# Kernel tuning notes

Hardware: AMD Instinct MI355X
Metric: run time of the kernel (lower is better)

Reference implementation:

```python
import jax, jax.numpy as jnp
import numpy as np

B = 8          # batch_size
N = 2048       # N_particles
D_SP = 2       # spatial dims
D = 16         # D_SP + hidden_dim
K = 32         # max_num_neighbors
R = 0.08       # neighbor_radius
DT = 0.01      # leapfrog step
BIG = 1e9


def setup_inputs() -> dict:
    key = jax.random.key(0)
    ks = jax.random.split(key, 8)
    H, C = 64, 32
    # node state: small random hidden features, deterministic disk positions
    x = jax.random.normal(ks[0], (B * N, D), dtype=jnp.float32) * 0.001
    i = jnp.arange(N, dtype=jnp.float32)
    golden = jnp.pi * (3.0 - jnp.sqrt(5.0))
    theta = i * golden
    r = 0.6 * jnp.sqrt((i + 0.5) / N)
    pos = jnp.stack([r * jnp.cos(theta), r * jnp.sin(theta)], axis=1)  # [N,2]
    pos = jnp.tile(pos, (B, 1)) + 0.01 * jax.random.normal(ks[1], (B * N, 2), dtype=jnp.float32)
    x = x.at[:, :D_SP].set(pos)
    W1 = jax.random.normal(ks[2], (2 * D, H), dtype=jnp.float32) * (1.0 / np.sqrt(2 * D))
    b1 = jnp.zeros((H,), jnp.float32)
    W2 = jax.random.normal(ks[3], (H, C), dtype=jnp.float32) * (1.0 / np.sqrt(H))
    b2 = jnp.zeros((C,), jnp.float32)
    Wout = jax.random.normal(ks[4], (C, 1), dtype=jnp.float32) * (1.0 / np.sqrt(C))
    bout = jnp.zeros((1,), jnp.float32)
    batch = jnp.repeat(jnp.arange(B, dtype=jnp.int64), N)
    return {"x": x, "W1": W1, "b1": b1, "W2": W2, "b2": b2,
            "Wout": Wout, "bout": bout, "batch": batch, "steps": 2}


def reference(x, W1, b1, W2, b2, Wout, bout, batch, steps):
    Bn, Df = x.shape
    Bc = int(np.asarray(batch)[-1]) + 1      # batch is contiguous blocks
    Nn = Bn // Bc
    eye = jnp.eye(Nn, dtype=x.dtype) * BIG   # no self-loops (loop=False)

    def hamiltonian(xv):
        xb = xv.reshape(Bc, Nn, Df)
        pos = xb[:, :, :D_SP]                              # [B,N,2]
        # radius_graph: pairwise sq-dist per simulation, capped at K neighbors
        d2 = jnp.sum((pos[:, :, None, :] - pos[:, None, :, :]) ** 2, axis=-1)  # [B,N,N]
        d2 = d2 + eye
        negd, idx = jax.lax.top_k(-d2, K)                  # K nearest per node
        valid = (-negd) < (R * R)                          # [B,N,K]
        # gather neighbor states (HNNConv message on concat(x_i, x_j))
        xj = xb[jnp.arange(Bc)[:, None, None], idx]        # [B,N,K,D]
        xi = jnp.broadcast_to(xb[:, :, None, :], xj.shape)
        m = jnp.tanh(jnp.concatenate([xi, xj], axis=-1) @ W1 + b1)  # [B,N,K,H]
        m = m @ W2 + b2                                    # [B,N,K,C]
        m = jnp.where(valid[..., None], m, 0.0)
        agg = m.sum(axis=2)                                # sum aggregation [B,N,C]
        h = agg @ Wout + bout                              # per-node Hamiltonian [B,N,1]
        return h.sum()

    for _ in range(int(steps)):
        dHdx = jax.grad(hamiltonian)(x)
        x = x - DT * dHdx
    return x
```

## Files before the change

kernel.cpp:

```cpp
#include <hip/hip_runtime.h>
#include <cstdint>
#include <cstddef>

#define BB   8
#define NN   2048
#define DD   16
#define HHH  64
#define KK   32
#define CAP  96
#define DT_C 0.01f
#define R2_C (0.08f * 0.08f)
#define CEXP (-2.885390081777927f)

#define WPB   16
#define BLOCK (WPB * 64)

__device__ __forceinline__ float dist2(float px, float py, float qx, float qy) {
    float dx = __fsub_rn(px, qx);
    float dy = __fsub_rn(py, qy);
    return __fadd_rn(__fmul_rn(dx, dx), __fmul_rn(dy, dy));
}

__device__ __forceinline__ int mbcnt64(unsigned long long m) {
    return (int)__builtin_amdgcn_mbcnt_hi(
        (unsigned)(m >> 32), __builtin_amdgcn_mbcnt_lo((unsigned)m, 0u));
}

__device__ __forceinline__ int swizzled_particle(int blk, int w, int& bbase) {
    int vb = blk & 7, vi = blk >> 3;
    bbase = vb << 11;
    return bbase + vi * WPB + w;
}

template <bool FIRST>
__global__ __launch_bounds__(BLOCK) void k_neighbors(
    const float* __restrict__ x, const float* __restrict__ pos,
    const float* __restrict__ W1,
    unsigned short* __restrict__ nbr, int* __restrict__ cntArr,
    float* __restrict__ cutArr,
    float* __restrict__ Aplane, float* __restrict__ Dplane) {
    __shared__ float sPos[2 * NN];
    __shared__ float sW1[2 * DD * HHH];
    __shared__ float2 sDJ[WPB][CAP];

    int tid = threadIdx.x;
    int w = tid >> 6, lane = tid & 63;
    int bbase;
    int p = swizzled_particle(blockIdx.x, w, bbase);
    int pl = p & (NN - 1);

    float2* sPos2w = (float2*)sPos;
    if (FIRST) {
        for (int t = tid; t < NN; t += BLOCK)
            sPos2w[t] = *(const float2*)(x + (size_t)(bbase + t) * DD);
    } else {
        for (int t = tid; t < 2 * NN; t += BLOCK) sPos[t] = pos[bbase * 2 + t];
    }
    for (int t = tid; t < 2 * DD * HHH; t += BLOCK) sW1[t] = W1[t];
    __syncthreads();

    float xv = (lane < DD) ? x[(size_t)p * DD + lane] : 0.f;
    float A = 0.f, Dv = 0.f;
#pragma unroll
    for (int f = 0; f < DD; f++) {
        float xf = __shfl(xv, f);
        A  = fmaf(xf, sW1[f * HHH + lane], A);
        Dv = fmaf(xf, sW1[(DD + f) * HHH + lane], Dv);
    }
    Aplane[((size_t)p << 6) + lane] = A;
    Dplane[((size_t)p << 6) + lane] = Dv;

    float px = sPos[2 * pl], py = sPos[2 * pl + 1];
    const float2* sPos2 = (const float2*)sPos;
    int cnt = 0;
    for (int c0 = 0; c0 < NN; c0 += 256) {
        float2 q[4];
#pragma unroll
        for (int u = 0; u < 4; ++u) q[u] = sPos2[c0 + (u << 6) + lane];
#pragma unroll
        for (int u = 0; u < 4; ++u) {
            int j = c0 + (u << 6) + lane;
            float d2 = dist2(px, py, q[u].x, q[u].y);
            bool hit = (d2 < R2_C) && (j != pl);
            unsigned long long m = __ballot(hit);
            int idx = cnt + mbcnt64(m & ((1ull << lane) - 1ull));
            if (hit && idx < CAP)
                sDJ[w][idx] = make_float2(d2, __uint_as_float((unsigned)j));
            cnt += (int)__popcll(m);
        }
    }
    if (cnt > CAP) cnt = CAP;
    __threadfence_block();

    float cutoff = R2_C;
    if (cnt > KK) {
        const float INF = 1e30f;
        if (cnt <= 64) {
            float v = (lane < cnt) ? sDJ[w][lane].x : INF;
#pragma unroll
            for (int k = 2; k <= 64; k <<= 1) {
#pragma unroll
                for (int j = k >> 1; j > 0; j >>= 1) {
                    float pv = __shfl_xor(v, j);
                    bool up = ((lane & k) == 0);
                    bool takeMin = (((lane & j) == 0) == up);
                    v = takeMin ? fminf(v, pv) : fmaxf(v, pv);
                }
            }
            cutoff = __shfl(v, KK - 1);
        } else {
            float e0 = (lane < cnt) ? sDJ[w][lane].x : INF;
            float e1 = (lane + 64 < cnt) ? sDJ[w][lane + 64].x : INF;
            int r0 = 0, q0 = 0, r1 = 0, q1 = 0;
            for (int k = 0; k < cnt; k++) {
                float val = sDJ[w][k].x;
                r0 += (val < e0); q0 += (val == e0);
                r1 += (val < e1); q1 += (val == e1);
            }
            bool c0 = (r0 <= KK - 1) && (r0 + q0 > KK - 1);
            bool c1 = (r1 <= KK - 1) && (r1 + q1 > KK - 1);
            float cand = c0 ? e0 : (c1 ? e1 : INF);
#pragma unroll
            for (int off = 32; off; off >>= 1) cand = fminf(cand, __shfl_xor(cand, off));
            cutoff = cand;
        }
    }
    if (lane == 0) { cutArr[p] = cutoff; cntArr[p] = cnt; }
    for (int c = lane; c < cnt; c += 64) {
        float2 e = sDJ[w][c];
        unsigned j = __float_as_uint(e.y);
        bool fwd = (e.x <= cutoff);
        nbr[(size_t)p * CAP + c] = (unsigned short)(j | (fwd ? 0x8000u : 0u));
    }
}

template <bool FIRST>
__global__ __launch_bounds__(BLOCK) void k_grad(
    const float* __restrict__ x, const float* __restrict__ pos,
    const float* __restrict__ cutArr, const int* __restrict__ cntArr,
    const unsigned short* __restrict__ nbr,
    const float* __restrict__ Aplane, const float* __restrict__ Dplane,
    const float* __restrict__ W1, const float* __restrict__ b1,
    const float* __restrict__ W2, const float* __restrict__ Wout,
    float* __restrict__ xOut, float* __restrict__ posOut) {
    __shared__ float sW1t[HHH * 33];
    __shared__ alignas(16) unsigned short sFwd[WPB][CAP];
    __shared__ alignas(16) unsigned short sRev[WPB][CAP];
    __shared__ float sS[WPB][128];
    __shared__ float sV[HHH];

    int tid = threadIdx.x;
    int w = tid >> 6, h = tid & 63;
    int bbase;
    int p = swizzled_particle(blockIdx.x, w, bbase);

    for (int t = tid; t < 2 * DD * HHH; t += BLOCK) {
        int f = t >> 6, hh = t & 63;
        sW1t[hh * 33 + f] = W1[t];
    }
    if (tid < HHH) {
        float acc = 0.f;
        for (int c = 0; c < 32; c++) acc = fmaf(W2[tid * 32 + c], Wout[c], acc);
        sV[tid] = acc;
    }
    __syncthreads();

    float b1h = b1[h];
    float Apb = Aplane[((size_t)p << 6) + h] + b1h;
    float Dpb = Dplane[((size_t)p << 6) + h] + b1h;
    float vh4 = 4.f * sV[h];
    int cnt = cntArr[p];

    float px, py;
    if (FIRST) {
        float2 pp = *(const float2*)(x + (size_t)p * DD);
        px = pp.x; py = pp.y;
    } else {
        float2 pp = *(const float2*)(pos + (size_t)p * 2);
        px = pp.x; py = pp.y;
    }

    int mf = 0, mr = 0;
    for (int c0 = 0; c0 < cnt; c0 += 64) {
        int c = c0 + h;
        bool act = c < cnt;
        int cc = act ? c : cnt - 1;
        int jp = (int)nbr[(size_t)p * CAP + cc];
        int jl = jp & (NN - 1);
        float2 q;
        if (FIRST) q = *(const float2*)(x + (size_t)(bbase + jl) * DD);
        else       q = *(const float2*)(pos + (size_t)(bbase + jl) * 2);
        float d2 = dist2(px, py, q.x, q.y);
        float cutj = cutArr[bbase + jl];
        bool fwd = act && (jp & 0x8000);
        bool rev = act && (d2 <= cutj);
        unsigned long long mF = __ballot(fwd);
        int iF = mf + mbcnt64(mF & ((1ull << h) - 1ull));
        if (fwd) sFwd[w][iF] = (unsigned short)jl;
        mf += (int)__popcll(mF);
        unsigned long long mR = __ballot(rev);
        int iR = mr + mbcnt64(mR & ((1ull << h) - 1ull));
        if (rev) sRev[w][iR] = (unsigned short)jl;
        mr += (int)__popcll(mR);
    }
    __threadfence_block();

    const float* baseD = Dplane + ((size_t)bbase << 6);
    const float* baseA = Aplane + ((size_t)bbase << 6);
    float T1 = 0.f, T2 = 0.f;

    auto s2core = [&](float z) {
        float a = __builtin_amdgcn_exp2f(CEXP * fabsf(z));
        float bb = 1.f + a;
        return a * __builtin_amdgcn_rcpf(bb * bb);
    };

#define UNPACK8(Q0, Q1, U)                                            \
    unsigned U[8];                                                    \
    U[0] = (unsigned)__builtin_amdgcn_readfirstlane(Q0.x);            \
    U[1] = (unsigned)__builtin_amdgcn_readfirstlane(Q0.y);            \
    U[2] = (unsigned)__builtin_amdgcn_readfirstlane(Q0.z);            \
    U[3] = (unsigned)__builtin_amdgcn_readfirstlane(Q0.w);            \
    U[4] = (unsigned)__builtin_amdgcn_readfirstlane(Q1.x);            \
    U[5] = (unsigned)__builtin_amdgcn_readfirstlane(Q1.y);            \
    U[6] = (unsigned)__builtin_amdgcn_readfirstlane(Q1.z);            \
    U[7] = (unsigned)__builtin_amdgcn_readfirstlane(Q1.w);

    {
        const unsigned short* L = sFwd[w];
        int c = 0;
        for (; c + 16 <= mf; c += 16) {
            int4 q0 = *(const int4*)(L + c);
            int4 q1 = *(const int4*)(L + c + 8);
            UNPACK8(q0, q1, u)
            float d[16];
#pragma unroll
            for (int k = 0; k < 8; ++k) {
                d[2 * k]     = baseD[((size_t)(u[k] & 0xffffu) << 6) + h];
                d[2 * k + 1] = baseD[((size_t)(u[k] >> 16) << 6) + h];
            }
#pragma unroll
            for (int k = 0; k < 16; ++k) T1 += s2core(Apb + d[k]);
        }
        for (; c + 8 <= mf; c += 8) {
            int4 q0 = *(const int4*)(L + c);
            int4 q1 = q0;
            UNPACK8(q0, q1, u)
            float d[8];
#pragma unroll
            for (int k = 0; k < 4; ++k) {
                d[2 * k]     = baseD[((size_t)(u[k] & 0xffffu) << 6) + h];
                d[2 * k + 1] = baseD[((size_t)(u[k] >> 16) << 6) + h];
            }
#pragma unroll
            for (int k = 0; k < 8; ++k) T1 += s2core(Apb + d[k]);
        }
        for (; c < mf; ++c) {
            unsigned jl = (unsigned)__builtin_amdgcn_readfirstlane((int)L[c]);
            T1 += s2core(Apb + baseD[((size_t)jl << 6) + h]);
        }
    }
    {
        const unsigned short* L = sRev[w];
        int c = 0;
        for (; c + 16 <= mr; c += 16) {
            int4 q0 = *(const int4*)(L + c);
            int4 q1 = *(const int4*)(L + c + 8);
            UNPACK8(q0, q1, u)
            float d[16];
#pragma unroll
            for (int k = 0; k < 8; ++k) {
                d[2 * k]     = baseA[((size_t)(u[k] & 0xffffu) << 6) + h];
                d[2 * k + 1] = baseA[((size_t)(u[k] >> 16) << 6) + h];
            }
#pragma unroll
            for (int k = 0; k < 16; ++k) T2 += s2core(Dpb + d[k]);
        }
        for (; c + 8 <= mr; c += 8) {
            int4 q0 = *(const int4*)(L + c);
            int4 q1 = q0;
            UNPACK8(q0, q1, u)
            float d[8];
#pragma unroll
            for (int k = 0; k < 4; ++k) {
                d[2 * k]     = baseA[((size_t)(u[k] & 0xffffu) << 6) + h];
                d[2 * k + 1] = baseA[((size_t)(u[k] >> 16) << 6) + h];
            }
#pragma unroll
            for (int k = 0; k < 8; ++k) T2 += s2core(Dpb + d[k]);
        }
        for (; c < mr; ++c) {
            unsigned jl = (unsigned)__builtin_amdgcn_readfirstlane((int)L[c]);
            T2 += s2core(Dpb + baseA[((size_t)jl << 6) + h]);
        }
    }
#undef UNPACK8

    sS[w][h] = vh4 * T1;
    sS[w][64 + h] = vh4 * T2;
    __threadfence_block();

    float g = 0.f;
    if (h < 32) {
        const float* Sv = &sS[w][(h < 16) ? 0 : 64];
        float acc = 0.f;
        for (int hh = 0; hh < 64; hh++) acc = fmaf(sW1t[hh * 33 + h], Sv[hh], acc);
        g = acc;
    }
    float g2 = __shfl(g, (h + 16) & 63);
    if (h < DD) {
        float xn = x[(size_t)p * DD + h] - DT_C * (g + g2);
        xOut[(size_t)p * DD + h] = xn;
        if (h < 2) posOut[p * 2 + h] = xn;
    }
}

extern "C" void kernel_launch(void* const* d_in, const int* in_sizes, int n_in,
                              void* d_out, int out_size, void* d_ws, size_t ws_size,
                              hipStream_t stream) {
    const float* x0   = (const float*)d_in[0];
    const float* W1   = (const float*)d_in[1];
    const float* b1   = (const float*)d_in[2];
    const float* W2   = (const float*)d_in[3];
    const float* Wout = (const float*)d_in[5];
    float* out = (float*)d_out;

    float* ws   = (float*)d_ws;
    float* posA = ws;
    float* posB = posA + 32768;
    float* x1   = posB + 32768;
    float* Apl  = x1 + 262144;
    float* Dpl  = Apl + 16384 * 64;
    float* cut  = Dpl + 16384 * 64;
    int*   cnt  = (int*)(cut + 16384);
    unsigned short* nbr = (unsigned short*)(cnt + 16384);

    dim3 blk(BLOCK);
    const int NBLK = (BB * NN) / WPB;

    k_neighbors<true><<<NBLK, blk, 0, stream>>>(x0, nullptr, W1, nbr, cnt, cut, Apl, Dpl);
    k_grad<true><<<NBLK, blk, 0, stream>>>(x0, nullptr, cut, cnt, nbr, Apl, Dpl,
                                           W1, b1, W2, Wout, x1, posB);
    k_neighbors<false><<<NBLK, blk, 0, stream>>>(x1, posB, W1, nbr, cnt, cut, Apl, Dpl);
    k_grad<false><<<NBLK, blk, 0, stream>>>(x1, posB, cut, cnt, nbr, Apl, Dpl,
                                            W1, b1, W2, Wout, out, posA);
}
```

Measured before the change: 178.3 us.

## Store candidate distances and compacted forward list to skip recomputation in grad kernel

The neighbor kernel now writes each candidate's (distance, index) pair and a compacted forward-neighbor list (capped at 48), and packs the forward count into the count array. The grad kernel no longer gathers neighbor positions or recomputes distances. It reads stored distances and compares them against the neighbor's cutoff to build the reverse list. The grad kernel's block size also drops from 16 to 8 waves. This trades extra global writes of float2 candidates for fewer scattered position loads and ballots in the grad kernel. Capping the forward list could drop neighbors if ties push the count above 48.

```diff
diff --git a/kernel.cpp b/kernel.cpp
--- a/kernel.cpp
+++ b/kernel.cpp
@@ -8,12 +8,15 @@
 #define HHH  64
 #define KK   32
 #define CAP  96
+#define FCAP 48
 #define DT_C 0.01f
 #define R2_C (0.08f * 0.08f)
 #define CEXP (-2.885390081777927f)
 
-#define WPB   16
-#define BLOCK (WPB * 64)
+#define WPB1  16
+#define BLK1  (WPB1 * 64)
+#define WPB2  8
+#define BLK2  (WPB2 * 64)
 
 __device__ __forceinline__ float dist2(float px, float py, float qx, float qy) {
     float dx = __fsub_rn(px, qx);
@@ -26,37 +29,37 @@
         (unsigned)(m >> 32), __builtin_amdgcn_mbcnt_lo((unsigned)m, 0u));
 }
 
-__device__ __forceinline__ int swizzled_particle(int blk, int w, int& bbase) {
+__device__ __forceinline__ int swizzled_particle(int blk, int wpb, int w, int& bbase) {
     int vb = blk & 7, vi = blk >> 3;
     bbase = vb << 11;
-    return bbase + vi * WPB + w;
+    return bbase + vi * wpb + w;
 }
 
 template <bool FIRST>
-__global__ __launch_bounds__(BLOCK) void k_neighbors(
+__global__ __launch_bounds__(BLK1) void k_neighbors(
     const float* __restrict__ x, const float* __restrict__ pos,
     const float* __restrict__ W1,
-    unsigned short* __restrict__ nbr, int* __restrict__ cntArr,
-    float* __restrict__ cutArr,
+    float2* __restrict__ candList, unsigned short* __restrict__ fwdList,
+    int* __restrict__ cntArr, float* __restrict__ cutArr,
     float* __restrict__ Aplane, float* __restrict__ Dplane) {
     __shared__ float sPos[2 * NN];
     __shared__ float sW1[2 * DD * HHH];
-    __shared__ float2 sDJ[WPB][CAP];
+    __shared__ float2 sDJ[WPB1][CAP];
 
     int tid = threadIdx.x;
     int w = tid >> 6, lane = tid & 63;
     int bbase;
-    int p = swizzled_particle(blockIdx.x, w, bbase);
+    int p = swizzled_particle(blockIdx.x, WPB1, w, bbase);
     int pl = p & (NN - 1);
 
     float2* sPos2w = (float2*)sPos;
     if (FIRST) {
-        for (int t = tid; t < NN; t += BLOCK)
+        for (int t = tid; t < NN; t += BLK1)
             sPos2w[t] = *(const float2*)(x + (size_t)(bbase + t) * DD);
     } else {
-        for (int t = tid; t < 2 * NN; t += BLOCK) sPos[t] = pos[bbase * 2 + t];
-    }
-    for (int t = tid; t < 2 * DD * HHH; t += BLOCK) sW1[t] = W1[t];
+        for (int t = tid; t < 2 * NN; t += BLK1) sPos[t] = pos[bbase * 2 + t];
+    }
+    for (int t = tid; t < 2 * DD * HHH; t += BLK1) sW1[t] = W1[t];
     __syncthreads();
 
     float xv = (lane < DD) ? x[(size_t)p * DD + lane] : 0.f;
@@ -125,36 +128,44 @@
             cutoff = cand;
         }
     }
-    if (lane == 0) { cutArr[p] = cutoff; cntArr[p] = cnt; }
-    for (int c = lane; c < cnt; c += 64) {
-        float2 e = sDJ[w][c];
-        unsigned j = __float_as_uint(e.y);
-        bool fwd = (e.x <= cutoff);
-        nbr[(size_t)p * CAP + c] = (unsigned short)(j | (fwd ? 0x8000u : 0u));
-    }
-}
-
-template <bool FIRST>
-__global__ __launch_bounds__(BLOCK) void k_grad(
-    const float* __restrict__ x, const float* __restrict__ pos,
+
+    int mf = 0;
+    for (int c0 = 0; c0 < cnt; c0 += 64) {
+        int c = c0 + lane;
+        bool act = c < cnt;
+        float2 e = sDJ[w][act ? c : 0];
+        if (act) candList[(size_t)p * CAP + c] = e;
+        bool fwd = act && (e.x <= cutoff);
+        unsigned long long mF = __ballot(fwd);
+        int iF = mf + mbcnt64(mF & ((1ull << lane) - 1ull));
+        if (fwd && iF < FCAP)
+            fwdList[(size_t)p * FCAP + iF] = (unsigned short)__float_as_uint(e.y);
+        mf += (int)__popcll(mF);
+    }
+    if (mf > FCAP) mf = FCAP;
+    if (lane == 0) { cutArr[p] = cutoff; cntArr[p] = cnt | (mf << 16); }
+}
+
+__global__ __launch_bounds__(BLK2) void k_grad(
+    const float* __restrict__ x,
     const float* __restrict__ cutArr, const int* __restrict__ cntArr,
-    const unsigned short* __restrict__ nbr,
+    const float2* __restrict__ candList, const unsigned short* __restrict__ fwdList,
     const float* __restrict__ Aplane, const float* __restrict__ Dplane,
     const float* __restrict__ W1, const float* __restrict__ b1,
     const float* __restrict__ W2, const float* __restrict__ Wout,
     float* __restrict__ xOut, float* __restrict__ posOut) {
     __shared__ float sW1t[HHH * 33];
-    __shared__ alignas(16) unsigned short sFwd[WPB][CAP];
-    __shared__ alignas(16) unsigned short sRev[WPB][CAP];
-    __shared__ float sS[WPB][128];
+    __shared__ alignas(16) unsigned short sFwd[WPB2][FCAP];
+    __shared__ alignas(16) unsigned short sRev[WPB2][CAP];
+    __shared__ float sS[WPB2][128];
     __shared__ float sV[HHH];
 
     int tid = threadIdx.x;
     int w = tid >> 6, h = tid & 63;
     int bbase;
-    int p = swizzled_particle(blockIdx.x, w, bbase);
-
-    for (int t = tid; t < 2 * DD * HHH; t += BLOCK) {
+    int p = swizzled_particle(blockIdx.x, WPB2, w, bbase);
+
+    for (int t = tid; t < 2 * DD * HHH; t += BLK2) {
         int f = t >> 6, hh = t & 63;
         sW1t[hh * 33 + f] = W1[t];
     }
@@ -169,35 +180,19 @@
     float Apb = Aplane[((size_t)p << 6) + h] + b1h;
     float Dpb = Dplane[((size_t)p << 6) + h] + b1h;
     float vh4 = 4.f * sV[h];
-    int cnt = cntArr[p];
-
-    float px, py;
-    if (FIRST) {
-        float2 pp = *(const float2*)(x + (size_t)p * DD);
-        px = pp.x; py = pp.y;
-    } else {
-        float2 pp = *(const float2*)(pos + (size_t)p * 2);
-        px = pp.x; py = pp.y;
-    }
-
-    int mf = 0, mr = 0;
+    int packed = cntArr[p];
+    int cnt = packed & 0xffff;
+    int mf = packed >> 16;
+
+    if (h < mf) sFwd[w][h] = fwdList[(size_t)p * FCAP + h];
+
+    int mr = 0;
     for (int c0 = 0; c0 < cnt; c0 += 64) {
         int c = c0 + h;
         bool act = c < cnt;
-        int cc = act ? c : cnt - 1;
-        int jp = (int)nbr[(size_t)p * CAP + cc];
-        int jl = jp & (NN - 1);
-        float2 q;
-        if (FIRST) q = *(const float2*)(x + (size_t)(bbase + jl) * DD);
-        else       q = *(const float2*)(pos + (size_t)(bbase + jl) * 2);
-        float d2 = dist2(px, py, q.x, q.y);
-        float cutj = cutArr[bbase + jl];
-        bool fwd = act && (jp & 0x8000);
-        bool rev = act && (d2 <= cutj);
-        unsigned long long mF = __ballot(fwd);
-        int iF = mf + mbcnt64(mF & ((1ull << h) - 1ull));
-        if (fwd) sFwd[w][iF] = (unsigned short)jl;
-        mf += (int)__popcll(mF);
+        float2 e = candList[(size_t)p * CAP + (act ? c : 0)];
+        unsigned jl = __float_as_uint(e.y) & (NN - 1);
+        bool rev = act && (e.x <= cutArr[bbase + jl]);
         unsigned long long mR = __ballot(rev);
         int iR = mr + mbcnt64(mR & ((1ull << h) - 1ull));
         if (rev) sRev[w][iR] = (unsigned short)jl;
@@ -333,15 +328,18 @@
     float* Dpl  = Apl + 16384 * 64;
     float* cut  = Dpl + 16384 * 64;
     int*   cnt  = (int*)(cut + 16384);
-    unsigned short* nbr = (unsigned short*)(cnt + 16384);
-
-    dim3 blk(BLOCK);
-    const int NBLK = (BB * NN) / WPB;
-
-    k_neighbors<true><<<NBLK, blk, 0, stream>>>(x0, nullptr, W1, nbr, cnt, cut, Apl, Dpl);
-    k_grad<true><<<NBLK, blk, 0, stream>>>(x0, nullptr, cut, cnt, nbr, Apl, Dpl,
-                                           W1, b1, W2, Wout, x1, posB);
-    k_neighbors<false><<<NBLK, blk, 0, stream>>>(x1, posB, W1, nbr, cnt, cut, Apl, Dpl);
-    k_grad<false><<<NBLK, blk, 0, stream>>>(x1, posB, cut, cnt, nbr, Apl, Dpl,
-                                            W1, b1, W2, Wout, out, posA);
-}
+    float2* cand = (float2*)(cnt + 16384);
+    unsigned short* fwd = (unsigned short*)(cand + (size_t)16384 * CAP);
+
+    const int NB1 = (BB * NN) / WPB1;
+    const int NB2 = (BB * NN) / WPB2;
+
+    k_neighbors<true><<<NB1, BLK1, 0, stream>>>(x0, nullptr, W1, cand, fwd, cnt, cut,
+                                                Apl, Dpl);
+    k_grad<<<NB2, BLK2, 0, stream>>>(x0, cut, cnt, cand, fwd, Apl, Dpl,
+                                     W1, b1, W2, Wout, x1, posB);
+    k_neighbors<false><<<NB1, BLK1, 0, stream>>>(x1, posB, W1, cand, fwd, cnt, cut,
+                                                 Apl, Dpl);
+    k_grad<<<NB2, BLK2, 0, stream>>>(x1, cut, cnt, cand, fwd, Apl, Dpl,
+                                     W1, b1, W2, Wout, out, posA);
+}
```

Measured after the change: 180.7 us. Within noise of the previous version (+1.3%).
